# Performance work log

Hardware: AMD Instinct MI355X
Metric: run time of the kernel (lower is better)

Reference implementation:

```python
import jax, jax.numpy as jnp
import numpy as np

DIM = 1024; HEADS = 16; HEAD = 64; FFN_H = 4096
LE = 8; TOPK = 2; DIM_E = 512; DIM_S = 1024
B = 1; S = 2048; N = B * S; NMOE = 2
THETA = 10000.0; EPS = 1e-6; RSF = 1.0


def rmsnorm(x, g):
    return x * jax.lax.rsqrt(jnp.mean(x * x, axis=-1, keepdims=True) + EPS) * g


def rotary(x):
    # x: [b, h, s, a]; matches RotaryEmb: split halves, y1=x1*cos+x2*sin, y2=-x1*sin+x2*cos
    a = x.shape[-1]; s = x.shape[2]
    inv_freq = (1.0 / THETA) ** (jnp.arange(0, a, 2, dtype=jnp.float32) / a)
    freqs = jnp.arange(s, dtype=jnp.float32)[:, None] * inv_freq[None, :]  # [s, a/2]
    cos, sin = jnp.cos(freqs), jnp.sin(freqs)
    x1, x2 = jnp.split(x, 2, axis=-1)
    return jnp.concatenate([x1 * cos + x2 * sin, -x1 * sin + x2 * cos], axis=-1)


def attention(x, attn_w, attn_o, doc):
    # causal + same-document masked attention (flex_attention mask_mod equivalent)
    b, s, d = x.shape
    xq, xk, xv = jnp.split(x @ attn_w, 3, axis=-1)
    def heads(t):
        return t.reshape(b, s, HEADS, HEAD).transpose(0, 2, 1, 3)
    xq, xk, xv = heads(xq), heads(xk), heads(xv)
    xq, xk = rotary(xq), rotary(xk)
    scores = jnp.einsum('bhqa,bhka->bhqk', xq, xk) / jnp.sqrt(jnp.float32(HEAD))
    q_idx = jnp.arange(s)
    mask = (q_idx[:, None] >= q_idx[None, :])[None] & (doc[:, :, None] == doc[:, None, :])
    scores = jnp.where(mask[:, None, :, :], scores, -jnp.inf)
    probs = jax.nn.softmax(scores, axis=-1)
    out = jnp.einsum('bhqk,bhka->bhqa', probs, xv)
    return out.transpose(0, 2, 1, 3).reshape(b, s, d) @ attn_o


def dense_layer(x, aw, ao, up, down, ag, fg, doc):
    xi = attention(rmsnorm(x, ag), aw, ao, doc) + x
    xf = rmsnorm(xi, fg)
    x1, x2 = jnp.split(xf @ up, 2, axis=-1)
    return (jax.nn.silu(x1) * x2) @ down + xi


def moe_layer(x, aw, ao, ag, fg, experts, tkeys, rbias, sup, sdown, idx, vals, doc):
    xi = attention(rmsnorm(x, ag), aw, ao, doc) + x
    xf = rmsnorm(xi, fg)                     # [b,s,d]
    flat = xf.reshape(-1, DIM)               # [N,d]
    # routing: base values + token-key logits + bias, sigmoid, renormalize
    tv = flat @ tkeys                        # [N,le]
    vals = vals + jnp.take_along_axis(tv, idx, axis=-1) + rbias[idx]
    sc = jax.nn.sigmoid(vals)
    sc = sc / jnp.sum(sc, axis=-1, keepdims=True) * RSF   # [N,k]
    # grouped-gemm experts (SwiGLU per expert); dense-over-experts then gather
    h1 = jnp.einsum('nd,edh->neh', flat, experts[0])
    h2 = jnp.einsum('nd,edh->neh', flat, experts[1])
    y_all = jnp.einsum('neh,edh->ned', jax.nn.silu(h1) * h2, experts[2])
    y_sel = jnp.take_along_axis(y_all, idx[:, :, None], axis=1)   # [N,k,d]
    y = jnp.sum(y_sel * sc[:, :, None], axis=1).reshape(xf.shape)
    # shared expert
    x1, x2 = jnp.split(xf @ sup, 2, axis=-1)
    y = y + (jax.nn.silu(x1) * x2) @ sdown
    return y + xi


def setup_inputs() -> dict:
    key = jax.random.key(0)
    ks = jax.random.split(key, 24)
    w = lambda k, shp: (jax.random.normal(k, shp, dtype=jnp.float32) * 0.02)
    inp = {
        'x': jax.random.normal(ks[0], (B, S, DIM), dtype=jnp.float32),
        'doc': jnp.sort(jax.random.randint(ks[1], (B, S), 0, 4), axis=-1).astype(jnp.int32),
        'indices': jax.random.randint(ks[2], (NMOE, N, TOPK), 0, LE).astype(jnp.int64),
        'values': jax.random.normal(ks[3], (NMOE, N, TOPK), dtype=jnp.float32),
        # 2 dense layers (first_k=1, last_k=1)
        'dense_attn_w': w(ks[4], (2, DIM, 3 * DIM)),
        'dense_attn_o': w(ks[5], (2, DIM, DIM)),
        'dense_ffn_up': w(ks[6], (2, DIM, 2 * FFN_H)),
        'dense_ffn_down': w(ks[7], (2, FFN_H, DIM)),
        'dense_attn_g': jnp.ones((2, DIM), dtype=jnp.float32),
        'dense_ffn_g': jnp.ones((2, DIM), dtype=jnp.float32),
        # 2 MoE layers
        'moe_attn_w': w(ks[8], (NMOE, DIM, 3 * DIM)),
        'moe_attn_o': w(ks[9], (NMOE, DIM, DIM)),
        'moe_attn_g': jnp.ones((NMOE, DIM), dtype=jnp.float32),
        'moe_ffn_g': jnp.ones((NMOE, DIM), dtype=jnp.float32),
        'moe_experts': w(ks[10], (NMOE, 3, LE, DIM, DIM_E)),
        'moe_token_keys': w(ks[11], (NMOE, DIM, LE)),
        'moe_router_bias': jnp.zeros((NMOE, LE), dtype=jnp.float32),
        'moe_shared_up': w(ks[12], (NMOE, DIM, 2 * DIM_S)),
        'moe_shared_down': w(ks[13], (NMOE, DIM_S, DIM)),
    }
    return inp


def reference(x, doc, indices, values, dense_attn_w, dense_attn_o, dense_ffn_up,
              dense_ffn_down, dense_attn_g, dense_ffn_g, moe_attn_w, moe_attn_o,
              moe_attn_g, moe_ffn_g, moe_experts, moe_token_keys, moe_router_bias,
              moe_shared_up, moe_shared_down):
    x = dense_layer(x, dense_attn_w[0], dense_attn_o[0], dense_ffn_up[0],
                    dense_ffn_down[0], dense_attn_g[0], dense_ffn_g[0], doc)
    for i in range(NMOE):
        x = moe_layer(x, moe_attn_w[i], moe_attn_o[i], moe_attn_g[i], moe_ffn_g[i],
                      moe_experts[i], moe_token_keys[i], moe_router_bias[i],
                      moe_shared_up[i], moe_shared_down[i], indices[i], values[i], doc)
    x = dense_layer(x, dense_attn_w[1], dense_attn_o[1], dense_ffn_up[1],
                    dense_ffn_down[1], dense_attn_g[1], dense_ffn_g[1], doc)
    return x
```

## Files before the change

### kernel.cpp

```cpp
#include <hip/hip_runtime.h>
#include <cmath>
#include <cstddef>
#include <cstdint>

#define DIMM   1024
#define HEADS  16
#define HEADD  64
#define FFN_H  4096
#define LE     8
#define TOPK   2
#define DIM_E  512
#define DIM_S  1024
#define NTOK   2048

typedef __bf16 bf16x8 __attribute__((ext_vector_type(8)));
typedef float  f32x4  __attribute__((ext_vector_type(4)));

union BF4 { __bf16 h[4]; uint2 u; };
union BF2 { __bf16 h[2]; uint32_t u; };

__device__ __forceinline__ void ldg_lds16(const __bf16* g, __bf16* l) {
    __builtin_amdgcn_global_load_lds(
        (const __attribute__((address_space(1))) uint32_t*)g,
        (__attribute__((address_space(3))) uint32_t*)l, 16, 0, 0);
}

__global__ __launch_bounds__(256) void rmsnorm_bf(
    const float* __restrict__ x, const float* __restrict__ g,
    __bf16* __restrict__ y)
{
    const int row = blockIdx.x;
    const int t = threadIdx.x;
    const float* xr = x + (size_t)row * DIMM;
    float4 v = *(const float4*)(xr + t * 4);
    float ss = v.x * v.x + v.y * v.y + v.z * v.z + v.w * v.w;
    #pragma unroll
    for (int off = 32; off > 0; off >>= 1) ss += __shfl_down(ss, off, 64);
    __shared__ float ws[4];
    if ((t & 63) == 0) ws[t >> 6] = ss;
    __syncthreads();
    const float tot = ws[0] + ws[1] + ws[2] + ws[3];
    const float scale = rsqrtf(tot * (1.0f / DIMM) + 1e-6f);
    const float4 gv = *(const float4*)(g + t * 4);
    BF4 o;
    o.h[0] = (__bf16)(v.x * scale * gv.x);
    o.h[1] = (__bf16)(v.y * scale * gv.y);
    o.h[2] = (__bf16)(v.z * scale * gv.z);
    o.h[3] = (__bf16)(v.w * scale * gv.w);
    *(uint2*)(y + (size_t)row * DIMM + t * 4) = o.u;
}

template <typename OutT>
__global__ __launch_bounds__(256) void gemm_bf_t(
    const __bf16* __restrict__ A, const __bf16* __restrict__ BT,
    const float* __restrict__ add, OutT* __restrict__ C,
    int M, int N, int K)
{
    __shared__ __bf16 As[128 * 32];
    __shared__ __bf16 Bs[128 * 32];
    const int t = threadIdx.x;
    const int m0 = blockIdx.y * 128, n0 = blockIdx.x * 128;
    const int lane = t & 63;
    const int wv = t >> 6;
    const int mw = (wv >> 1) * 64, nw = (wv & 1) * 64;
    const int fr = lane & 15;
    const int fk = ((lane >> 4) ^ ((fr >> 1) & 3)) * 8;
    const int r0 = t >> 2;
    const int q0l = (t & 3) * 8;
    const int q0s = ((t & 3) ^ ((t >> 3) & 3)) * 8;

    const __bf16* gA0 = A + (size_t)(m0 + r0) * K + q0s;
    const __bf16* gA1 = A + (size_t)(m0 + 64 + r0) * K + q0s;
    const __bf16* gB0 = BT + (size_t)(n0 + r0) * K + q0s;
    const __bf16* gB1 = BT + (size_t)(n0 + 64 + r0) * K + q0s;
    __bf16* lA0 = &As[r0 * 32 + q0l];
    __bf16* lA1 = &As[(64 + r0) * 32 + q0l];
    __bf16* lB0 = &Bs[r0 * 32 + q0l];
    __bf16* lB1 = &Bs[(64 + r0) * 32 + q0l];

    f32x4 acc[4][4];
    #pragma unroll
    for (int i = 0; i < 4; ++i)
        #pragma unroll
        for (int j = 0; j < 4; ++j) acc[i][j] = (f32x4){0.f, 0.f, 0.f, 0.f};

    for (int k0 = 0; k0 < K; k0 += 32) {
        __syncthreads();
        ldg_lds16(gA0 + k0, lA0);
        ldg_lds16(gA1 + k0, lA1);
        ldg_lds16(gB0 + k0, lB0);
        ldg_lds16(gB1 + k0, lB1);
        __syncthreads();
        bf16x8 af[4], bfr[4];
        #pragma unroll
        for (int i = 0; i < 4; ++i) {
            af[i]  = *(const bf16x8*)&As[(mw + i * 16 + fr) * 32 + fk];
            bfr[i] = *(const bf16x8*)&Bs[(nw + i * 16 + fr) * 32 + fk];
        }
        #pragma unroll
        for (int i = 0; i < 4; ++i)
            #pragma unroll
            for (int j = 0; j < 4; ++j)
                acc[i][j] = __builtin_amdgcn_mfma_f32_16x16x32_bf16(
                    af[i], bfr[j], acc[i][j], 0, 0, 0);
    }
    const int cn = lane & 15, cr = (lane >> 4) * 4;
    #pragma unroll
    for (int i = 0; i < 4; ++i)
        #pragma unroll
        for (int j = 0; j < 4; ++j)
            #pragma unroll
            for (int r = 0; r < 4; ++r) {
                const size_t off = (size_t)(m0 + mw + i * 16 + cr + r) * N
                                 + (n0 + nw + j * 16 + cn);
                if constexpr (__is_same(OutT, float))
                    C[off] = acc[i][j][r] + (add ? add[off] : 0.f);
                else
                    C[off] = (__bf16)acc[i][j][r];
            }
}

__global__ __launch_bounds__(256) void gemm_bf_splitk(
    const __bf16* __restrict__ A, const __bf16* __restrict__ BT,
    float* __restrict__ P, int M, int N, int K, int KS)
{
    __shared__ __bf16 As[128 * 32];
    __shared__ __bf16 Bs[128 * 32];
    const int t = threadIdx.x;
    const int m0 = blockIdx.y * 128, n0 = blockIdx.x * 128;
    const int kz0 = blockIdx.z * KS;
    const int lane = t & 63;
    const int wv = t >> 6;
    const int mw = (wv >> 1) * 64, nw = (wv & 1) * 64;
    const int fr = lane & 15;
    const int fk = ((lane >> 4) ^ ((fr >> 1) & 3)) * 8;
    const int r0 = t >> 2;
    const int q0l = (t & 3) * 8;
    const int q0s = ((t & 3) ^ ((t >> 3) & 3)) * 8;

    const __bf16* gA0 = A + (size_t)(m0 + r0) * K + q0s;
    const __bf16* gA1 = A + (size_t)(m0 + 64 + r0) * K + q0s;
    const __bf16* gB0 = BT + (size_t)(n0 + r0) * K + q0s;
    const __bf16* gB1 = BT + (size_t)(n0 + 64 + r0) * K + q0s;
    __bf16* lA0 = &As[r0 * 32 + q0l];
    __bf16* lA1 = &As[(64 + r0) * 32 + q0l];
    __bf16* lB0 = &Bs[r0 * 32 + q0l];
    __bf16* lB1 = &Bs[(64 + r0) * 32 + q0l];

    f32x4 acc[4][4];
    #pragma unroll
    for (int i = 0; i < 4; ++i)
        #pragma unroll
        for (int j = 0; j < 4; ++j) acc[i][j] = (f32x4){0.f, 0.f, 0.f, 0.f};

    for (int k0 = kz0; k0 < kz0 + KS; k0 += 32) {
        __syncthreads();
        ldg_lds16(gA0 + k0, lA0);
        ldg_lds16(gA1 + k0, lA1);
        ldg_lds16(gB0 + k0, lB0);
        ldg_lds16(gB1 + k0, lB1);
        __syncthreads();
        bf16x8 af[4], bfr[4];
        #pragma unroll
        for (int i = 0; i < 4; ++i) {
            af[i]  = *(const bf16x8*)&As[(mw + i * 16 + fr) * 32 + fk];
            bfr[i] = *(const bf16x8*)&Bs[(nw + i * 16 + fr) * 32 + fk];
        }
        #pragma unroll
        for (int i = 0; i < 4; ++i)
            #pragma unroll
            for (int j = 0; j < 4; ++j)
                acc[i][j] = __builtin_amdgcn_mfma_f32_16x16x32_bf16(
                    af[i], bfr[j], acc[i][j], 0, 0, 0);
    }
    float* Pz = P + (size_t)blockIdx.z * M * N;
    const int cn = lane & 15, cr = (lane >> 4) * 4;
    #pragma unroll
    for (int i = 0; i < 4; ++i)
        #pragma unroll
        for (int j = 0; j < 4; ++j)
            #pragma unroll
            for (int r = 0; r < 4; ++r) {
                const size_t off = (size_t)(m0 + mw + i * 16 + cr + r) * N
                                 + (n0 + nw + j * 16 + cn);
                Pz[off] = acc[i][j][r];
            }
}

__global__ __launch_bounds__(256) void gemm_glu(
    const __bf16* __restrict__ A, const __bf16* __restrict__ BT,
    const float* __restrict__ sc, __bf16* __restrict__ G,
    int M, int Nout, int K, int pairOff)
{
    __shared__ __bf16 As[128 * 32];
    __shared__ __bf16 Bs[128 * 32];
    const int t = threadIdx.x;
    const int m0 = blockIdx.y * 128;
    const int b  = blockIdx.x;
    const int lane = t & 63;
    const int wv = t >> 6;
    const int mw = (wv >> 1) * 64, nw = (wv & 1) * 64;
    const int fr = lane & 15;
    const int fk = ((lane >> 4) ^ ((fr >> 1) & 3)) * 8;
    const int r0 = t >> 2;
    const int q0l = (t & 3) * 8;
    const int q0s = ((t & 3) ^ ((t >> 3) & 3)) * 8;

    const int grow0 = b * 64 + ((r0 >> 6) ? 32 : 0) + (r0 & 31)
                    + ((r0 >> 5) & 1) * pairOff;
    const int grow1 = grow0 + 32;

    const __bf16* gA0 = A + (size_t)(m0 + r0) * K + q0s;
    const __bf16* gA1 = A + (size_t)(m0 + 64 + r0) * K + q0s;
    const __bf16* gB0 = BT + (size_t)grow0 * K + q0s;
    const __bf16* gB1 = BT + (size_t)grow1 * K + q0s;
    __bf16* lA0 = &As[r0 * 32 + q0l];
    __bf16* lA1 = &As[(64 + r0) * 32 + q0l];
    __bf16* lB0 = &Bs[r0 * 32 + q0l];
    __bf16* lB1 = &Bs[(64 + r0) * 32 + q0l];

    f32x4 acc[4][4];
    #pragma unroll
    for (int i = 0; i < 4; ++i)
        #pragma unroll
        for (int j = 0; j < 4; ++j) acc[i][j] = (f32x4){0.f, 0.f, 0.f, 0.f};

    for (int k0 = 0; k0 < K; k0 += 32) {
        __syncthreads();
        ldg_lds16(gA0 + k0, lA0);
        ldg_lds16(gA1 + k0, lA1);
        ldg_lds16(gB0 + k0, lB0);
        ldg_lds16(gB1 + k0, lB1);
        __syncthreads();
        bf16x8 af[4], bfr[4];
        #pragma unroll
        for (int i = 0; i < 4; ++i) {
            af[i]  = *(const bf16x8*)&As[(mw + i * 16 + fr) * 32 + fk];
            bfr[i] = *(const bf16x8*)&Bs[(nw + i * 16 + fr) * 32 + fk];
        }
        #pragma unroll
        for (int i = 0; i < 4; ++i)
            #pragma unroll
            for (int j = 0; j < 4; ++j)
                acc[i][j] = __builtin_amdgcn_mfma_f32_16x16x32_bf16(
                    af[i], bfr[j], acc[i][j], 0, 0, 0);
    }
    const int cn = lane & 15, cr = (lane >> 4) * 4;
    const int e = (b * 64) >> 9;
    #pragma unroll
    for (int i = 0; i < 4; ++i)
        #pragma unroll
        for (int r = 0; r < 4; ++r) {
            const int m = m0 + mw + i * 16 + cr + r;
            const float s = sc ? sc[m * LE + e] : 1.f;
            #pragma unroll
            for (int j = 0; j < 2; ++j) {
                const float h1 = acc[i][j][r];
                const float h2 = acc[i][j + 2][r];
                const float o = (h1 / (1.f + __expf(-h1))) * h2 * s;
                const int col = b * 64 + (nw >> 1) + j * 16 + cn;
                G[(size_t)m * Nout + col] = (__bf16)o;
            }
        }
}

__global__ __launch_bounds__(256) void reduce4_add(
    const float* __restrict__ P, const float* __restrict__ add,
    float* __restrict__ out, size_t MN)
{
    const size_t i = ((size_t)blockIdx.x * 256 + threadIdx.x) * 4;
    float4 s  = *(const float4*)(P + i);
    const float4 s1 = *(const float4*)(P + MN + i);
    const float4 s2 = *(const float4*)(P + 2 * MN + i);
    const float4 s3 = *(const float4*)(P + 3 * MN + i);
    const float4 a  = *(const float4*)(add + i);
    s.x += s1.x + s2.x + s3.x + a.x;
    s.y += s1.y + s2.y + s3.y + a.y;
    s.z += s1.z + s2.z + s3.z + a.z;
    s.w += s1.w + s2.w + s3.w + a.w;
    *(float4*)(out + i) = s;
}

__global__ __launch_bounds__(256) void reduce2_add(
    const float* __restrict__ P, const float* __restrict__ add,
    float* __restrict__ out, size_t MN)
{
    const size_t i = ((size_t)blockIdx.x * 256 + threadIdx.x) * 4;
    float4 s  = *(const float4*)(P + i);
    const float4 s1 = *(const float4*)(P + MN + i);
    const float4 a  = *(const float4*)(add + i);
    s.x += s1.x + a.x;
    s.y += s1.y + a.y;
    s.z += s1.z + a.z;
    s.w += s1.w + a.w;
    *(float4*)(out + i) = s;
}

__global__ __launch_bounds__(256) void transpose_cast(
    const float* __restrict__ in, __bf16* __restrict__ out, int R, int C)
{
    __shared__ float tile[32][33];
    const int bx = blockIdx.x * 32, by = blockIdx.y * 32;
    const size_t bz = (size_t)blockIdx.z * R * C;
    const int tx = threadIdx.x & 31, ty = threadIdx.x >> 5;
    const float* ip = in + bz;
    __bf16* op = out + bz;
    #pragma unroll
    for (int i = 0; i < 4; ++i)
        tile[ty + i * 8][tx] = ip[(size_t)(by + ty + i * 8) * C + bx + tx];
    __syncthreads();
    #pragma unroll
    for (int i = 0; i < 4; ++i)
        op[(size_t)(bx + ty + i * 8) * R + by + tx] = (__bf16)tile[tx][ty + i * 8];
}

__global__ __launch_bounds__(256) void cast_w2(
    const float* __restrict__ in, __bf16* __restrict__ out)
{
    const int i = blockIdx.x * 256 + threadIdx.x;
    const int d = i >> 12, r = i & 4095;
    const int e = r >> 9, h = r & 511;
    out[i] = (__bf16)in[(size_t)e * (DIMM * DIM_E) + d * DIM_E + h];
}

__global__ __launch_bounds__(256) void rotary_kernel(float* __restrict__ qkv)
{
    const int i = blockIdx.x * 256 + threadIdx.x;
    const int s = i >> 9;
    const int rem = i & 511;
    const int h = rem >> 5;
    const int j = rem & 31;
    const float inv_freq = __expf(-(float)j * (9.210340371976184f / 32.f));
    const float f = (float)s * inv_freq;
    float sn, cs;
    sincosf(f, &sn, &cs);
    float* base = qkv + (size_t)s * 3072 + h * 64 + j;
    const float q1 = base[0], q2 = base[32];
    base[0]  = q1 * cs + q2 * sn;
    base[32] = -q1 * sn + q2 * cs;
    const float k1 = base[1024], k2 = base[1024 + 32];
    base[1024]      = k1 * cs + k2 * sn;
    base[1024 + 32] = -k1 * sn + k2 * cs;
}

#define KS_STRIDE 72
#define VT_STRIDE 72
#define PW_STRIDE 36
#define LOG2E 1.4426950408889634f

__global__ __launch_bounds__(256) void attn_mfma(
    const float* __restrict__ qkv, const int* __restrict__ doc,
    __bf16* __restrict__ out)
{
    const int h = blockIdx.x;
    const int qb = blockIdx.y;
    const int t = threadIdx.x;
    const int wv = t >> 6, lane = t & 63;
    const int l15 = lane & 15, lhi = lane >> 4;
    const int q0w = qb * 64 + wv * 16;

    __shared__ __bf16 Ks[64 * KS_STRIDE];
    __shared__ __bf16 Vt[64 * VT_STRIDE];
    __shared__ float  Pw[4][16 * PW_STRIDE];
    __shared__ int    docs[64];

    bf16x8 qf[2];
    {
        const float* qrow = qkv + (size_t)(q0w + l15) * 3072 + h * 64 + lhi * 8;
        #pragma unroll
        for (int db = 0; db < 2; ++db) {
            const float4 v0 = *(const float4*)(qrow + db * 32);
            const float4 v1 = *(const float4*)(qrow + db * 32 + 4);
            bf16x8 f;
            f[0] = (__bf16)(v0.x * 0.125f); f[1] = (__bf16)(v0.y * 0.125f);
            f[2] = (__bf16)(v0.z * 0.125f); f[3] = (__bf16)(v0.w * 0.125f);
            f[4] = (__bf16)(v1.x * 0.125f); f[5] = (__bf16)(v1.y * 0.125f);
            f[6] = (__bf16)(v1.z * 0.125f); f[7] = (__bf16)(v1.w * 0.125f);
            qf[db] = f;
        }
    }
    int myDoc[4];
    #pragma unroll
    for (int rg = 0; rg < 4; ++rg) myDoc[rg] = doc[q0w + lhi * 4 + rg];

    float mrow[4] = {-INFINITY, -INFINITY, -INFINITY, -INFINITY};
    float lrow[4] = {0.f, 0.f, 0.f, 0.f};
    f32x4 oacc[4];
    #pragma unroll
    for (int nb = 0; nb < 4; ++nb) oacc[nb] = (f32x4){0.f, 0.f, 0.f, 0.f};

    const int docQ0 = doc[qb * 64];
    const int ntiles = qb + 1;

    for (int kt = 0; kt < ntiles; ++kt) {
        if (doc[kt * 64 + 63] < docQ0) continue;
        __syncthreads();
        {
            const int key = t >> 2, dof = (t & 3) * 16;
            const float* kr = qkv + (size_t)(kt * 64 + key) * 3072 + 1024 + h * 64 + dof;
            float kv[16];
            *(float4*)&kv[0]  = *(const float4*)(kr + 0);
            *(float4*)&kv[4]  = *(const float4*)(kr + 4);
            *(float4*)&kv[8]  = *(const float4*)(kr + 8);
            *(float4*)&kv[12] = *(const float4*)(kr + 12);
            bf16x8 p0, p1;
            #pragma unroll
            for (int j = 0; j < 8; ++j) { p0[j] = (__bf16)kv[j]; p1[j] = (__bf16)kv[8 + j]; }
            *(bf16x8*)&Ks[key * KS_STRIDE + dof] = p0;
            *(bf16x8*)&Ks[key * KS_STRIDE + dof + 8] = p1;
            const int k2 = (t & 31) * 2, df = (t >> 5) * 8;
            const float* vr0 = qkv + (size_t)(kt * 64 + k2) * 3072 + 2048 + h * 64 + df;
            float va[8], vb[8];
            *(float4*)&va[0] = *(const float4*)(vr0 + 0);
            *(float4*)&va[4] = *(const float4*)(vr0 + 4);
            *(float4*)&vb[0] = *(const float4*)(vr0 + 3072);
            *(float4*)&vb[4] = *(const float4*)(vr0 + 3076);
            #pragma unroll
            for (int d = 0; d < 8; ++d) {
                BF2 wpk;
                wpk.h[0] = (__bf16)va[d];
                wpk.h[1] = (__bf16)vb[d];
                *(uint32_t*)&Vt[(df + d) * VT_STRIDE + k2] = wpk.u;
            }
            if (t < 64) docs[t] = doc[kt * 64 + t];
        }
        __syncthreads();

        #pragma unroll
        for (int g = 0; g < 2; ++g) {
            f32x4 s[2];
            #pragma unroll
            for (int sg = 0; sg < 2; ++sg) {
                const int keyloc = g * 32 + sg * 16;
                const bf16x8 kf0 = *(const bf16x8*)&Ks[(keyloc + l15) * KS_STRIDE + lhi * 8];
                const bf16x8 kf1 = *(const bf16x8*)&Ks[(keyloc + l15) * KS_STRIDE + 32 + lhi * 8];
                f32x4 a = (f32x4){0.f, 0.f, 0.f, 0.f};
                a = __builtin_amdgcn_mfma_f32_16x16x32_bf16(qf[0], kf0, a, 0, 0, 0);
                a = __builtin_amdgcn_mfma_f32_16x16x32_bf16(qf[1], kf1, a, 0, 0, 0);
                s[sg] = a;
            }
            float sv0[4], sv1[4], cmax[4];
            #pragma unroll
            for (int rg = 0; rg < 4; ++rg) {
                const int r = q0w + lhi * 4 + rg;
                const int key0 = kt * 64 + g * 32 + l15;
                const bool v0 = (key0 <= r) && (docs[g * 32 + l15] == myDoc[rg]);
                const bool v1 = (key0 + 16 <= r) && (docs[g * 32 + 16 + l15] == myDoc[rg]);
                sv0[rg] = v0 ? s[0][rg] : -INFINITY;
                sv1[rg] = v1 ? s[1][rg] : -INFINITY;
                cmax[rg] = fmaxf(sv0[rg], sv1[rg]);
            }
            #pragma unroll
            for (int off = 1; off < 16; off <<= 1)
                #pragma unroll
                for (int rg = 0; rg < 4; ++rg)
                    cmax[rg] = fmaxf(cmax[rg], __shfl_xor(cmax[rg], off, 64));
            float alpha[4], p0[4], p1[4], rsum[4];
            #pragma unroll
            for (int rg = 0; rg < 4; ++rg) {
                const float mn = fmaxf(mrow[rg], cmax[rg]);
                alpha[rg] = (mn == -INFINITY) ? 1.f : exp2f((mrow[rg] - mn) * LOG2E);
                p0[rg] = (sv0[rg] == -INFINITY) ? 0.f : exp2f((sv0[rg] - mn) * LOG2E);
                p1[rg] = (sv1[rg] == -INFINITY) ? 0.f : exp2f((sv1[rg] - mn) * LOG2E);
                rsum[rg] = p0[rg] + p1[rg];
                mrow[rg] = mn;
            }
            #pragma unroll
            for (int off = 1; off < 16; off <<= 1)
                #pragma unroll
                for (int rg = 0; rg < 4; ++rg)
                    rsum[rg] += __shfl_xor(rsum[rg], off, 64);
            #pragma unroll
            for (int rg = 0; rg < 4; ++rg)
                lrow[rg] = lrow[rg] * alpha[rg] + rsum[rg];
            #pragma unroll
            for (int nb = 0; nb < 4; ++nb)
                #pragma unroll
                for (int rg = 0; rg < 4; ++rg)
                    oacc[nb][rg] *= alpha[rg];
            float* pp = &Pw[wv][0];
            #pragma unroll
            for (int rg = 0; rg < 4; ++rg) {
                pp[(lhi * 4 + rg) * PW_STRIDE + l15] = p0[rg];
                pp[(lhi * 4 + rg) * PW_STRIDE + 16 + l15] = p1[rg];
            }
            const f32x4 pa = *(const f32x4*)&pp[l15 * PW_STRIDE + lhi * 8];
            const f32x4 pb = *(const f32x4*)&pp[l15 * PW_STRIDE + lhi * 8 + 4];
            bf16x8 pf;
            pf[0] = (__bf16)pa[0]; pf[1] = (__bf16)pa[1];
            pf[2] = (__bf16)pa[2]; pf[3] = (__bf16)pa[3];
            pf[4] = (__bf16)pb[0]; pf[5] = (__bf16)pb[1];
            pf[6] = (__bf16)pb[2]; pf[7] = (__bf16)pb[3];
            #pragma unroll
            for (int nb = 0; nb < 4; ++nb) {
                const bf16x8 vf = *(const bf16x8*)&Vt[(nb * 16 + l15) * VT_STRIDE + g * 32 + lhi * 8];
                oacc[nb] = __builtin_amdgcn_mfma_f32_16x16x32_bf16(pf, vf, oacc[nb], 0, 0, 0);
            }
        }
    }
    float inv[4];
    #pragma unroll
    for (int rg = 0; rg < 4; ++rg) inv[rg] = 1.f / lrow[rg];
    #pragma unroll
    for (int nb = 0; nb < 4; ++nb)
        #pragma unroll
        for (int rg = 0; rg < 4; ++rg)
            out[(size_t)(q0w + lhi * 4 + rg) * DIMM + h * 64 + nb * 16 + l15] =
                (__bf16)(oacc[nb][rg] * inv[rg]);
}

__global__ __launch_bounds__(64) void router_bf(
    const __bf16* __restrict__ xf, const float* __restrict__ tkeys,
    const float* __restrict__ rbias, const int* __restrict__ idx,
    const float* __restrict__ vals, float* __restrict__ sc)
{
    const int n = blockIdx.x;
    const int t = threadIdx.x;
    const int e0 = idx[n * 2 + 0], e1 = idx[n * 2 + 1];
    float a0 = 0.f, a1 = 0.f;
    for (int d = t; d < DIMM; d += 64) {
        const float xv = (float)xf[(size_t)n * DIMM + d];
        a0 += xv * tkeys[d * LE + e0];
        a1 += xv * tkeys[d * LE + e1];
    }
    #pragma unroll
    for (int off = 32; off > 0; off >>= 1) {
        a0 += __shfl_down(a0, off, 64);
        a1 += __shfl_down(a1, off, 64);
    }
    if (t == 0) {
        const float v0 = vals[n * 2 + 0] + a0 + rbias[e0];
        const float v1 = vals[n * 2 + 1] + a1 + rbias[e1];
        const float s0 = 1.f / (1.f + __expf(-v0));
        const float s1 = 1.f / (1.f + __expf(-v1));
        const float inv = 1.f / (s0 + s1);
        float r[LE];
        #pragma unroll
        for (int e = 0; e < LE; ++e) r[e] = 0.f;
        r[e0] += s0 * inv;
        r[e1] += s1 * inv;
        #pragma unroll
        for (int e = 0; e < LE; ++e) sc[n * LE + e] = r[e];
    }
}

struct Scratch {
    float *qkv, *xi, *t1, *sc, *xA, *xB, *part;
    __bf16 *xn_bf, *attnO_bf, *xf_bf, *wbuf, *gact_bf, *gs_bf;
};

static void attn_block(const float* x_in, const __bf16* awT, const __bf16* aoT,
                       const float* ag, const int* doc, Scratch& w, hipStream_t s)
{
    rmsnorm_bf<<<NTOK, 256, 0, s>>>(x_in, ag, w.xn_bf);
    gemm_bf_t<float><<<dim3(24, 16), 256, 0, s>>>(w.xn_bf, awT, nullptr, w.qkv, NTOK, 3072, 1024);
    rotary_kernel<<<(NTOK * 512) / 256, 256, 0, s>>>(w.qkv);
    attn_mfma<<<dim3(HEADS, NTOK / 64), 256, 0, s>>>(w.qkv, doc, w.attnO_bf);
    gemm_bf_splitk<<<dim3(8, 16, 2), 256, 0, s>>>(w.attnO_bf, aoT, w.qkv, NTOK, 1024, 1024, 512);
    reduce2_add<<<(NTOK * 1024) / 1024, 256, 0, s>>>(w.qkv, x_in, w.xi, (size_t)NTOK * 1024);
}

static void dense_layer_run(const float* x_in, float* x_out,
                            const float* aw, const float* ao,
                            const float* up, const float* down,
                            const float* ag, const float* fg,
                            const int* doc, Scratch& w, hipStream_t s)
{
    __bf16* awT = w.wbuf;
    __bf16* aoT = w.wbuf + 3145728;
    __bf16* upT = w.wbuf + 4194304;
    __bf16* dnT = w.wbuf + 12582912;
    transpose_cast<<<dim3(96, 32, 1), 256, 0, s>>>(aw, awT, 1024, 3072);
    transpose_cast<<<dim3(32, 32, 1), 256, 0, s>>>(ao, aoT, 1024, 1024);
    transpose_cast<<<dim3(256, 32, 1), 256, 0, s>>>(up, upT, 1024, 8192);
    transpose_cast<<<dim3(32, 128, 1), 256, 0, s>>>(down, dnT, 4096, 1024);
    attn_block(x_in, awT, aoT, ag, doc, w, s);
    rmsnorm_bf<<<NTOK, 256, 0, s>>>(w.xi, fg, w.xf_bf);
    gemm_glu<<<dim3(64, 16), 256, 0, s>>>(w.xf_bf, upT, nullptr, w.gact_bf, NTOK, 4096, 1024, 4096);
    gemm_bf_splitk<<<dim3(8, 16, 4), 256, 0, s>>>(w.gact_bf, dnT, w.part, NTOK, 1024, 4096, 1024);
    reduce4_add<<<(NTOK * 1024) / 1024, 256, 0, s>>>(w.part, w.xi, x_out, (size_t)NTOK * 1024);
}

static void moe_layer_run(const float* x_in, float* x_out,
                          const float* aw, const float* ao,
                          const float* ag, const float* fg,
                          const float* experts, const float* tkeys,
                          const float* rbias, const float* sup,
                          const float* sdn, const int* idx, const float* vals,
                          const int* doc, Scratch& w, hipStream_t s)
{
    __bf16* awT  = w.wbuf;
    __bf16* aoT  = w.wbuf + 3145728;
    __bf16* w01T = w.wbuf + 4194304;
    __bf16* w2c  = w.wbuf + 12582912;
    __bf16* supT = w.wbuf + 16777216;
    __bf16* sdnT = w.wbuf + 18874368;
    const size_t EW = (size_t)LE * DIMM * DIM_E;
    transpose_cast<<<dim3(96, 32, 1), 256, 0, s>>>(aw, awT, 1024, 3072);
    transpose_cast<<<dim3(32, 32, 1), 256, 0, s>>>(ao, aoT, 1024, 1024);
    transpose_cast<<<dim3(16, 32, 8), 256, 0, s>>>(experts, w01T, 1024, 512);
    transpose_cast<<<dim3(16, 32, 8), 256, 0, s>>>(experts + EW, w01T + 4194304, 1024, 512);
    cast_w2<<<16384, 256, 0, s>>>(experts + 2 * EW, w2c);
    transpose_cast<<<dim3(64, 32, 1), 256, 0, s>>>(sup, supT, 1024, 2048);
    transpose_cast<<<dim3(32, 32, 1), 256, 0, s>>>(sdn, sdnT, 1024, 1024);

    attn_block(x_in, awT, aoT, ag, doc, w, s);
    rmsnorm_bf<<<NTOK, 256, 0, s>>>(w.xi, fg, w.xf_bf);
    router_bf<<<NTOK, 64, 0, s>>>(w.xf_bf, tkeys, rbias, idx, vals, w.sc);
    gemm_glu<<<dim3(64, 16), 256, 0, s>>>(w.xf_bf, w01T, w.sc, w.gact_bf, NTOK, 4096, 1024, 4096);
    gemm_glu<<<dim3(16, 16), 256, 0, s>>>(w.xf_bf, supT, nullptr, w.gs_bf, NTOK, 1024, 1024, 1024);
    gemm_bf_splitk<<<dim3(8, 16, 2), 256, 0, s>>>(w.gs_bf, sdnT, w.part, NTOK, 1024, 1024, 512);
    reduce2_add<<<(NTOK * 1024) / 1024, 256, 0, s>>>(w.part, w.xi, w.t1, (size_t)NTOK * 1024);
    gemm_bf_splitk<<<dim3(8, 16, 4), 256, 0, s>>>(w.gact_bf, w2c, w.part, NTOK, 1024, 4096, 1024);
    reduce4_add<<<(NTOK * 1024) / 1024, 256, 0, s>>>(w.part, w.t1, x_out, (size_t)NTOK * 1024);
}

extern "C" void kernel_launch(void* const* d_in, const int* in_sizes, int n_in,
                              void* d_out, int out_size, void* d_ws, size_t ws_size,
                              hipStream_t stream)
{
    (void)in_sizes; (void)n_in; (void)out_size; (void)ws_size;
    const float* x       = (const float*)d_in[0];
    const int*   doc     = (const int*)d_in[1];
    const int*   indices = (const int*)d_in[2];
    const float* values  = (const float*)d_in[3];
    const float* d_aw    = (const float*)d_in[4];
    const float* d_ao    = (const float*)d_in[5];
    const float* d_up    = (const float*)d_in[6];
    const float* d_down  = (const float*)d_in[7];
    const float* d_ag    = (const float*)d_in[8];
    const float* d_fg    = (const float*)d_in[9];
    const float* m_aw    = (const float*)d_in[10];
    const float* m_ao    = (const float*)d_in[11];
    const float* m_ag    = (const float*)d_in[12];
    const float* m_fg    = (const float*)d_in[13];
    const float* m_ex    = (const float*)d_in[14];
    const float* m_tk    = (const float*)d_in[15];
    const float* m_rb    = (const float*)d_in[16];
    const float* m_sup   = (const float*)d_in[17];
    const float* m_sdn   = (const float*)d_in[18];

    Scratch w;
    float* f = (float*)d_ws;
    w.qkv = f; f += 6291456;
    w.xi  = f; f += 2097152;
    float* h12 = f; f += 16777216;
    w.t1  = h12 + 8388608;
    w.sc  = f; f += 16384;
    w.xA  = f; f += 2097152;
    w.xB  = f; f += 2097152;
    __bf16* b = (__bf16*)f;
    w.xn_bf    = b; b += 2097152;
    w.attnO_bf = b; b += 2097152;
    w.xf_bf    = b; b += 2097152;
    w.wbuf     = b; b += 19922944;
    w.gact_bf  = (__bf16*)w.qkv;
    w.gs_bf    = (__bf16*)w.qkv + 8388608;
    w.part     = h12;

    float* out = (float*)d_out;

    dense_layer_run(x, w.xA, d_aw, d_ao, d_up, d_down, d_ag, d_fg, doc, w, stream);
    const size_t EXL = (size_t)3 * LE * DIMM * DIM_E;
    moe_layer_run(w.xA, w.xB,
                  m_aw, m_ao, m_ag, m_fg,
                  m_ex, m_tk, m_rb, m_sup, m_sdn,
                  indices, values, doc, w, stream);
    moe_layer_run(w.xB, w.xA,
                  m_aw + (size_t)DIMM * 3 * DIMM, m_ao + (size_t)DIMM * DIMM,
                  m_ag + DIMM, m_fg + DIMM,
                  m_ex + EXL, m_tk + DIMM * LE, m_rb + LE,
                  m_sup + (size_t)DIMM * 2 * DIM_S, m_sdn + (size_t)DIM_S * DIMM,
                  indices + (size_t)NTOK * TOPK, values + (size_t)NTOK * TOPK,
                  doc, w, stream);
    dense_layer_run(w.xA, out,
                    d_aw + (size_t)DIMM * 3 * DIMM, d_ao + (size_t)DIMM * DIMM,
                    d_up + (size_t)DIMM * 2 * FFN_H, d_down + (size_t)FFN_H * DIMM,
                    d_ag + DIMM, d_fg + DIMM, doc, w, stream);
}
```

Before: 1.325 ms.

## Add 256x256-tile GLU GEMM with 4-stage LDS pipeline for large up-projections

Adds a new GLU GEMM kernel that uses 512 threads and 256x256 output tiles (128 GLU output columns) with a four-buffer global-to-LDS prefetch pipeline and explicit vmcnt waits. It replaces the 128-row tile GLU GEMM for the 4096-wide dense and expert up-projections. The aim is to raise arithmetic intensity per block and hide load latency behind deeper prefetch. In exchange, register and LDS pressure grow (128 KB of LDS, 32 accumulators per thread), and the grid shrinks to 256 blocks, which may limit occupancy.

```diff
diff --git a/kernel.cpp b/kernel.cpp
--- a/kernel.cpp
+++ b/kernel.cpp
@@ -259,6 +259,111 @@
                 const float h2 = acc[i][j + 2][r];
                 const float o = (h1 / (1.f + __expf(-h1))) * h2 * s;
                 const int col = b * 64 + (nw >> 1) + j * 16 + cn;
+                G[(size_t)m * Nout + col] = (__bf16)o;
+            }
+        }
+}
+
+__global__ __launch_bounds__(512, 2) void gemm_glu256(
+    const __bf16* __restrict__ A, const __bf16* __restrict__ BT,
+    const float* __restrict__ sc, __bf16* __restrict__ G,
+    int M, int Nout, int K, int pairOff)
+{
+    __shared__ __bf16 As[4][256 * 32];
+    __shared__ __bf16 Bs[4][256 * 32];
+    const int t = threadIdx.x;
+    const int m0 = blockIdx.y * 256;
+    const int b  = blockIdx.x;
+    const int lane = t & 63;
+    const int wv = t >> 6;
+    const int wr = wv >> 2, wc = wv & 3;
+    const int fr = lane & 15;
+    const int fk = ((lane >> 4) ^ ((fr >> 1) & 3)) * 8;
+
+    const int r0 = t >> 2;
+    const int c  = t & 3;
+    const int cs = (c ^ ((r0 >> 1) & 3)) * 8;
+    const int ldst = r0 * 32 + c * 8;
+
+    const int rem0 = r0 & 63;
+    const int grow0 = b * 128 + (r0 >> 6) * 32 + ((rem0 >> 4) & 1) * 16
+                    + (rem0 & 15) + (rem0 >> 5) * pairOff;
+    const int r1 = r0 + 128;
+    const int rem1 = r1 & 63;
+    const int grow1 = b * 128 + (r1 >> 6) * 32 + ((rem1 >> 4) & 1) * 16
+                    + (rem1 & 15) + (rem1 >> 5) * pairOff;
+
+    const __bf16* gA0 = A + (size_t)(m0 + r0) * K + cs;
+    const __bf16* gA1 = A + (size_t)(m0 + 128 + r0) * K + cs;
+    const __bf16* gB0 = BT + (size_t)grow0 * K + cs;
+    const __bf16* gB1 = BT + (size_t)grow1 * K + cs;
+
+    const int NT = K >> 5;
+
+#define STAGE256(bi, kt) do {                                   \
+        const int _k = (kt) << 5;                               \
+        ldg_lds16(gA0 + _k, &As[bi][ldst]);                     \
+        ldg_lds16(gA1 + _k, &As[bi][128 * 32 + ldst]);          \
+        ldg_lds16(gB0 + _k, &Bs[bi][ldst]);                     \
+        ldg_lds16(gB1 + _k, &Bs[bi][128 * 32 + ldst]);          \
+    } while (0)
+
+    f32x4 acc[8][4];
+    #pragma unroll
+    for (int i = 0; i < 8; ++i)
+        #pragma unroll
+        for (int j = 0; j < 4; ++j) acc[i][j] = (f32x4){0.f, 0.f, 0.f, 0.f};
+
+    STAGE256(0, 0);
+    STAGE256(1, 1);
+    STAGE256(2, 2);
+    asm volatile("s_waitcnt vmcnt(8)" ::: "memory");
+    __builtin_amdgcn_s_barrier();
+    asm volatile("" ::: "memory");
+
+    for (int kt = 0; kt < NT; ++kt) {
+        const int bi = kt & 3;
+        if (kt + 3 < NT) STAGE256((kt + 3) & 3, kt + 3);
+
+        bf16x8 af[8], bf[4];
+        const __bf16* Ab = &As[bi][(wr * 128 + fr) * 32 + fk];
+        #pragma unroll
+        for (int i = 0; i < 8; ++i) af[i] = *(const bf16x8*)(Ab + i * 16 * 32);
+        const __bf16* Bb = &Bs[bi][(wc * 64 + fr) * 32 + fk];
+        #pragma unroll
+        for (int j = 0; j < 4; ++j) bf[j] = *(const bf16x8*)(Bb + j * 16 * 32);
+
+        #pragma unroll
+        for (int i = 0; i < 8; ++i)
+            #pragma unroll
+            for (int j = 0; j < 4; ++j)
+                acc[i][j] = __builtin_amdgcn_mfma_f32_16x16x32_bf16(
+                    af[i], bf[j], acc[i][j], 0, 0, 0);
+
+        if (kt < NT - 1) {
+            if (kt < NT - 3)       asm volatile("s_waitcnt vmcnt(8)" ::: "memory");
+            else if (kt == NT - 3) asm volatile("s_waitcnt vmcnt(4)" ::: "memory");
+            else                   asm volatile("s_waitcnt vmcnt(0)" ::: "memory");
+            __builtin_amdgcn_s_barrier();
+            asm volatile("" ::: "memory");
+        }
+    }
+#undef STAGE256
+
+    const int cn = lane & 15, cr = (lane >> 4) * 4;
+    const int e = b >> 2;
+    #pragma unroll
+    for (int i = 0; i < 8; ++i)
+        #pragma unroll
+        for (int r = 0; r < 4; ++r) {
+            const int m = m0 + wr * 128 + i * 16 + cr + r;
+            const float s = sc ? sc[m * LE + e] : 1.f;
+            #pragma unroll
+            for (int j = 0; j < 2; ++j) {
+                const float h1 = acc[i][j][r];
+                const float h2 = acc[i][j + 2][r];
+                const float o = (h1 / (1.f + __expf(-h1))) * h2 * s;
+                const int col = b * 128 + wc * 32 + j * 16 + cn;
                 G[(size_t)m * Nout + col] = (__bf16)o;
             }
         }
@@ -576,7 +681,7 @@
     transpose_cast<<<dim3(32, 128, 1), 256, 0, s>>>(down, dnT, 4096, 1024);
     attn_block(x_in, awT, aoT, ag, doc, w, s);
     rmsnorm_bf<<<NTOK, 256, 0, s>>>(w.xi, fg, w.xf_bf);
-    gemm_glu<<<dim3(64, 16), 256, 0, s>>>(w.xf_bf, upT, nullptr, w.gact_bf, NTOK, 4096, 1024, 4096);
+    gemm_glu256<<<dim3(32, 8), 512, 0, s>>>(w.xf_bf, upT, nullptr, w.gact_bf, NTOK, 4096, 1024, 4096);
     gemm_bf_splitk<<<dim3(8, 16, 4), 256, 0, s>>>(w.gact_bf, dnT, w.part, NTOK, 1024, 4096, 1024);
     reduce4_add<<<(NTOK * 1024) / 1024, 256, 0, s>>>(w.part, w.xi, x_out, (size_t)NTOK * 1024);
 }
@@ -607,7 +712,7 @@
     attn_block(x_in, awT, aoT, ag, doc, w, s);
     rmsnorm_bf<<<NTOK, 256, 0, s>>>(w.xi, fg, w.xf_bf);
     router_bf<<<NTOK, 64, 0, s>>>(w.xf_bf, tkeys, rbias, idx, vals, w.sc);
-    gemm_glu<<<dim3(64, 16), 256, 0, s>>>(w.xf_bf, w01T, w.sc, w.gact_bf, NTOK, 4096, 1024, 4096);
+    gemm_glu256<<<dim3(32, 8), 512, 0, s>>>(w.xf_bf, w01T, w.sc, w.gact_bf, NTOK, 4096, 1024, 4096);
     gemm_glu<<<dim3(16, 16), 256, 0, s>>>(w.xf_bf, supT, nullptr, w.gs_bf, NTOK, 1024, 1024, 1024);
     gemm_bf_splitk<<<dim3(8, 16, 2), 256, 0, s>>>(w.gs_bf, sdnT, w.part, NTOK, 1024, 1024, 512);
     reduce2_add<<<(NTOK * 1024) / 1024, 256, 0, s>>>(w.part, w.xi, w.t1, (size_t)NTOK * 1024);
```

Result: faster. 1.296 ms (-2.2%).
